# Performance work log

Hardware: AMD Instinct MI355X
Metric: run time of the kernel (lower is better)

Reference implementation:

```python
import jax, jax.numpy as jnp
import numpy as np

T, B, V, L = 512, 32, 512, 128
NEG = -1e9  # safe -inf surrogate (keeps logaddexp gradients finite)


def setup_inputs() -> dict:
    key = jax.random.key(0)
    k1, k2, k3 = jax.random.split(key, 3)
    log_probs = jax.nn.log_softmax(
        jax.random.normal(k1, (T, B, V), dtype=jnp.float32), axis=-1)
    # ASG transition parameter (init ones in the module; use small noise for a
    # non-degenerate reference). transition[i, j] = score of j -> i.
    transition = 0.1 * jax.random.normal(k2, (V, V), dtype=jnp.float32)
    targets = jax.random.randint(k3, (B, L), 0, V)
    input_lengths = jnp.full((B,), T, dtype=jnp.int32)
    target_lengths = jnp.full((B,), L, dtype=jnp.int32)
    return {"log_probs": log_probs, "transition": transition,
            "targets": targets, "input_lengths": input_lengths,
            "target_lengths": target_lengths}


def _fcc(log_probs, transition, input_lengths):
    """Fully-connected criterion: log-partition over all label paths. [B]"""
    def step(alpha, lp_t):  # alpha, lp_t: [B, V]
        # alpha'[b, i] = lp_t[b, i] + logsumexp_j(alpha[b, j] + trans[i, j])
        alpha = lp_t + jax.nn.logsumexp(
            alpha[:, None, :] + transition[None, :, :], axis=2)
        return alpha, jax.nn.logsumexp(alpha, axis=1)

    a0 = log_probs[0]
    _, tail = jax.lax.scan(step, a0, log_probs[1:])
    scores = jnp.concatenate(
        [jax.nn.logsumexp(a0, axis=1)[None], tail], axis=0)  # [T, B]
    return scores[input_lengths - 1, jnp.arange(scores.shape[1])]


def _fac(log_probs, transition, targets, input_lengths, target_lengths):
    """Forced-alignment criterion: DP constrained to the target label seq. [B]"""
    Tt, Bb, _ = log_probs.shape
    Ll = targets.shape[1]
    trans_self = transition[targets, targets]                    # [B, L] stay
    trans_prev = transition[targets[:, 1:], targets[:, :-1]]     # [B, L-1] advance
    # emit[t, b, s] = log_probs[t, b, targets[b, s]]
    emit = jnp.take_along_axis(
        log_probs, jnp.broadcast_to(targets[None], (Tt, Bb, Ll)), axis=2)

    sel = (target_lengths - 1)[:, None]  # [B, 1]

    def final_of(beta):
        return jnp.take_along_axis(beta, sel, axis=1)[:, 0]

    beta0 = jnp.where(jnp.arange(Ll)[None, :] == 0, emit[0], NEG)  # [B, L]

    def step(beta, em_t):
        stay = beta + trans_self
        move = jnp.concatenate(
            [jnp.full((Bb, 1), NEG, beta.dtype),
             beta[:, :-1] + trans_prev], axis=1)
        beta = em_t + jnp.logaddexp(stay, move)
        return beta, final_of(beta)

    _, tail = jax.lax.scan(step, beta0, emit[1:])
    fins = jnp.concatenate([final_of(beta0)[None], tail], axis=0)  # [T, B]
    return fins[input_lengths - 1, jnp.arange(Bb)]


def reference(log_probs, transition, targets, input_lengths, target_lengths):
    # ASG loss (reduction='none'): FCC - FAC, shape [B]
    fcc = _fcc(log_probs, transition, input_lengths)
    fac = _fac(log_probs, transition, targets, input_lengths, target_lengths)
    return fcc - fac
```

## Files before the change

### kernel.cpp

```cpp
#include <hip/hip_runtime.h>
#include <stdint.h>

#define T_ 512
#define B_ 32
#define V_ 512
#define L_ 128
#define NEGF (-1000000000.0f)

#define SE_Q 69.0f
#define SU_Q 127.0f
#define LOGC 9.078313f

typedef int v4i __attribute__((ext_vector_type(4)));

template <int CTRL>
__device__ __forceinline__ int dppmov(int old_, int src) {
    return __builtin_amdgcn_update_dpp(old_, src, CTRL, 0xF, 0xF, false);
}
__device__ __forceinline__ float wave_max64(float x) {
    int xi = __float_as_int(x);
    x = fmaxf(x, __int_as_float(dppmov<0x111>(xi, xi))); xi = __float_as_int(x);
    x = fmaxf(x, __int_as_float(dppmov<0x112>(xi, xi))); xi = __float_as_int(x);
    x = fmaxf(x, __int_as_float(dppmov<0x114>(xi, xi))); xi = __float_as_int(x);
    x = fmaxf(x, __int_as_float(dppmov<0x118>(xi, xi))); xi = __float_as_int(x);
    x = fmaxf(x, __int_as_float(dppmov<0x142>(xi, xi))); xi = __float_as_int(x);
    x = fmaxf(x, __int_as_float(dppmov<0x143>(xi, xi)));
    return x;
}
__device__ __forceinline__ float wave_sum64(float x) {
    int xi = __float_as_int(x);
    x = x + __int_as_float(dppmov<0x111>(xi, xi)); xi = __float_as_int(x);
    x = x + __int_as_float(dppmov<0x112>(xi, xi)); xi = __float_as_int(x);
    x = x + __int_as_float(dppmov<0x114>(xi, xi)); xi = __float_as_int(x);
    x = x + __int_as_float(dppmov<0x118>(xi, xi)); xi = __float_as_int(x);
    x = x + __int_as_float(dppmov<0x142>(xi, xi)); xi = __float_as_int(x);
    x = x + __int_as_float(dppmov<0x143>(xi, xi));
    return x;
}
__device__ __forceinline__ unsigned fkey(float f) {
    unsigned u = __float_as_uint(f);
    return (u & 0x80000000u) ? ~u : (u | 0x80000000u);
}
__device__ __forceinline__ float funkey(unsigned k) {
    unsigned u = (k & 0x80000000u) ? (k ^ 0x80000000u) : ~k;
    return __uint_as_float(u);
}
__device__ __forceinline__ int sel4(v4i a, int r) {
    int x0 = (r & 1) ? a.y : a.x;
    int x1 = (r & 1) ? a.w : a.z;
    return (r & 2) ? x1 : x0;
}

__global__ void asg_prep(const float* __restrict__ trans, uint32_t* __restrict__ Et) {
    int o = blockIdx.x * blockDim.x + threadIdx.x;
    int d    = o & 3;
    int tid  = (o >> 2) & 511;
    int qreg = o >> 11;
    int tt = qreg >> 3, kt = qreg & 7;
    int w = tid >> 6, lane = tid & 63;
    int q = lane >> 4, n = lane & 15;
    int m  = 64 * w + 16 * tt + n;
    int k0 = 64 * kt + 16 * q + 4 * d;
    const float* tp = trans + (size_t)m * V_ + k0;
    uint32_t q0 = (uint32_t)fminf(127.0f, __expf(tp[0]) * SE_Q + 0.5f);
    uint32_t q1 = (uint32_t)fminf(127.0f, __expf(tp[1]) * SE_Q + 0.5f);
    uint32_t q2 = (uint32_t)fminf(127.0f, __expf(tp[2]) * SE_Q + 0.5f);
    uint32_t q3 = (uint32_t)fminf(127.0f, __expf(tp[3]) * SE_Q + 0.5f);
    Et[(size_t)o] = q0 | (q1 << 8) | (q2 << 16) | (q3 << 24);
}

__global__ __attribute__((amdgpu_flat_work_group_size(512, 512),
                          amdgpu_waves_per_eu(2, 2)))
void asg_main(
    const float* __restrict__ lp, const uint32_t* __restrict__ Et,
    const float* __restrict__ trans, const int* __restrict__ targets,
    const int* __restrict__ ilen, const int* __restrict__ tlen,
    float* __restrict__ fcc_ws, float* __restrict__ fac_ws)
{
    __shared__ float facb[256];
    __shared__ __align__(16) uint32_t u_lds[128];
    __shared__ __align__(16) float mw_lds[8];
    __shared__ unsigned mslotE;
    __shared__ float sumf;

    const int bb  = blockIdx.x;
    const int tid = threadIdx.x;

    if (bb < B_) {
        const int b    = bb;
        const int lane = tid & 63;
        const int w    = tid >> 6;
        const int q    = lane >> 4;
        const int n    = lane & 15;
        const int tt_o = n >> 2;
        const int rg_o = n & 3;
        const int i    = 64 * w + 16 * tt_o + 4 * q + rg_o;
        const int Tlen = ilen[b];

        uint4 er4[32];
        {
            const uint4* Eq = (const uint4*)Et;
            #pragma unroll
            for (int t8 = 0; t8 < 32; ++t8) er4[t8] = Eq[t8 * 512 + tid];
        }

        float lpv0 = lp[(size_t)b * V_ + i];
        float elp  = __expf(lpv0);
        float lpv  = lp[(size_t)(B_ * V_) + (size_t)b * V_ + i];
        float accf = 1.0f;
        float S    = 0.0f;
        if (tid == 0) { mslotE = 0u; sumf = 0.0f; }
        __syncthreads();

        for (int t = 1; t < Tlen; ++t) {
            float key   = elp * accf;
            float elp_n = __expf(lpv);

            {
                float mx = wave_max64(key);
                if (lane == 63) mw_lds[w] = mx;
            }
            __syncthreads();

            float4 m0 = *(const float4*)&mw_lds[0];
            float4 m1 = *(const float4*)&mw_lds[4];
            float kmax = fmaxf(fmaxf(fmaxf(m0.x, m0.y), fmaxf(m0.z, m0.w)),
                               fmaxf(fmaxf(m1.x, m1.y), fmaxf(m1.z, m1.w)));
            float r127 = 127.0f * __builtin_amdgcn_rcpf(kmax);

            {
                uint32_t qu = (uint32_t)fminf(127.0f, fmaf(key, r127, 0.5f));
                int pv = (int)(qu << (8 * (i & 3)));
                pv |= dppmov<0xB1>(pv, pv);
                pv |= dppmov<0x4E>(pv, pv);
                if ((i & 3) == 0) u_lds[i >> 2] = (uint32_t)pv;
            }
            __syncthreads();

            uint4 bf[8];
            #pragma unroll
            for (int kt = 0; kt < 8; ++kt)
                bf[kt] = *(const uint4*)((const char*)u_lds + 64 * kt + 16 * q);

            int tn = (t + 1 < Tlen) ? (t + 1) : t;
            float lpv_n = lp[(size_t)tn * (B_ * V_) + (size_t)b * V_ + i];

            v4i a0, a1, a2, a3;
            {
                v4i z = {0, 0, 0, 0};
                a0 = z; a1 = z; a2 = z; a3 = z;
            }
            #pragma unroll
            for (int kt = 0; kt < 8; ++kt) {
                v4i bv = __builtin_bit_cast(v4i, bf[kt]);
                a0 = __builtin_amdgcn_mfma_i32_16x16x64_i8(
                        __builtin_bit_cast(v4i, er4[0 * 8 + kt]), bv, a0, 0, 0, 0);
                a1 = __builtin_amdgcn_mfma_i32_16x16x64_i8(
                        __builtin_bit_cast(v4i, er4[1 * 8 + kt]), bv, a1, 0, 0, 0);
                a2 = __builtin_amdgcn_mfma_i32_16x16x64_i8(
                        __builtin_bit_cast(v4i, er4[2 * 8 + kt]), bv, a2, 0, 0, 0);
                a3 = __builtin_amdgcn_mfma_i32_16x16x64_i8(
                        __builtin_bit_cast(v4i, er4[3 * 8 + kt]), bv, a3, 0, 0, 0);
            }

            int s0 = sel4(a0, rg_o), s1 = sel4(a1, rg_o);
            int s2 = sel4(a2, rg_o), s3 = sel4(a3, rg_o);
            int y0 = (tt_o & 1) ? s1 : s0;
            int y1 = (tt_o & 1) ? s3 : s2;
            int acc = (tt_o & 2) ? y1 : y0;

            accf = (float)acc;
            S += __logf(kmax) - LOGC;
            elp = elp_n;
            lpv = lpv_n;
        }

        float alpha = ((Tlen > 1) ? lpv : lpv0) + S + __logf(accf);
        {
            float mx = wave_max64(alpha);
            if (lane == 63) atomicMax(&mslotE, fkey(mx));
        }
        __syncthreads();
        float m2 = funkey(mslotE);
        {
            float sv = wave_sum64(__expf(alpha - m2));
            if (lane == 63) atomicAdd(&sumf, sv);
        }
        __syncthreads();
        if (tid == 0) fcc_ws[b] = m2 + __logf(sumf);
    } else {
        const int b = bb - B_;
        const int l = tid;
        const bool active = (l < L_);
        const int Tlen = ilen[b];
        const int Llen = tlen[b];

        const int tl  = active ? targets[b * L_ + l] : 0;
        const int tlm = (active && l > 0) ? targets[b * L_ + l - 1] : 0;
        const float ts = active ? trans[(size_t)tl * V_ + tl] : 0.0f;
        const float tp = (active && l > 0) ? trans[(size_t)tl * V_ + tlm] : 0.0f;

        float beta = (l == 0) ? lp[(size_t)b * V_ + tl] : NEGF;
        float em_next = active ? lp[(size_t)1 * (B_ * V_) + (size_t)b * V_ + tl] : 0.0f;

        for (int t = 1; t < Tlen; ++t) {
            float* buf = facb + (t & 1) * L_;
            if (active) buf[l] = beta;
            __syncthreads();
            float prev = (active && l > 0) ? buf[l - 1] : NEGF;
            float em = em_next;
            if (active && t + 1 < Tlen)
                em_next = lp[(size_t)(t + 1) * (B_ * V_) + (size_t)b * V_ + tl];
            if (active) {
                float st = beta + ts;
                float mv = prev + tp;
                float mx = fmaxf(st, mv);
                float mn = fminf(st, mv);
                beta = em + mx + log1pf(__expf(mn - mx));
            }
        }
        if (active && l == Llen - 1) fac_ws[b] = beta;
    }
}

__global__ void asg_combine(const float* __restrict__ fcc_ws,
                            const float* __restrict__ fac_ws,
                            float* __restrict__ out) {
    int i = threadIdx.x;
    if (i < B_) out[i] = fcc_ws[i] - fac_ws[i];
}

extern "C" void kernel_launch(void* const* d_in, const int* in_sizes, int n_in,
                              void* d_out, int out_size, void* d_ws, size_t ws_size,
                              hipStream_t stream) {
    const float* lp      = (const float*)d_in[0];
    const float* trans   = (const float*)d_in[1];
    const int*   targets = (const int*)d_in[2];
    const int*   ilen    = (const int*)d_in[3];
    const int*   tlen    = (const int*)d_in[4];
    float* out = (float*)d_out;

    uint32_t* Et     = (uint32_t*)d_ws;
    float*    fcc_ws = (float*)((char*)d_ws + 65536 * 4);
    float*    fac_ws = fcc_ws + B_;

    hipLaunchKernelGGL(asg_prep, dim3(256), dim3(256), 0, stream, trans, Et);
    hipLaunchKernelGGL(asg_main, dim3(2 * B_), dim3(512), 0, stream,
                       lp, Et, trans, targets, ilen, tlen, fcc_ws, fac_ws);
    hipLaunchKernelGGL(asg_combine, dim3(1), dim3(64), 0, stream, fcc_ws, fac_ws, out);
}
```

Before: 558.7 us.

## Rotate K-tile order per wave and feed own tile via bpermute before barrier

Each wave now processes the K-tiles in a rotated order starting with its own tile. That first tile's B-operand is built directly from registers with ds_bpermute, so the first MFMAs can issue without waiting on the LDS round-trip of the other tiles. The exp of the next log-prob is moved later to overlap with the loads. The aim is to shorten the per-timestep critical path of the serial recurrence, at the cost of extra bpermute instructions and a rotated preload of the E registers.

Measured after the change: 577.7 us. +3.4%, slower.

```diff
diff --git a/kernel.cpp b/kernel.cpp
--- a/kernel.cpp
+++ b/kernel.cpp
@@ -101,7 +101,10 @@
         {
             const uint4* Eq = (const uint4*)Et;
             #pragma unroll
-            for (int t8 = 0; t8 < 32; ++t8) er4[t8] = Eq[t8 * 512 + tid];
+            for (int tt = 0; tt < 4; ++tt)
+                #pragma unroll
+                for (int s = 0; s < 8; ++s)
+                    er4[tt * 8 + s] = Eq[(tt * 8 + ((w + s) & 7)) * 512 + tid];
         }
 
         float lpv0 = lp[(size_t)b * V_ + i];
@@ -113,8 +116,7 @@
         __syncthreads();
 
         for (int t = 1; t < Tlen; ++t) {
-            float key   = elp * accf;
-            float elp_n = __expf(lpv);
+            float key = elp * accf;
 
             {
                 float mx = wave_max64(key);
@@ -128,39 +130,60 @@
                                fmaxf(fmaxf(m1.x, m1.y), fmaxf(m1.z, m1.w)));
             float r127 = 127.0f * __builtin_amdgcn_rcpf(kmax);
 
+            int pv;
             {
                 uint32_t qu = (uint32_t)fminf(127.0f, fmaf(key, r127, 0.5f));
-                int pv = (int)(qu << (8 * (i & 3)));
+                pv = (int)(qu << (8 * (i & 3)));
                 pv |= dppmov<0xB1>(pv, pv);
                 pv |= dppmov<0x4E>(pv, pv);
                 if ((i & 3) == 0) u_lds[i >> 2] = (uint32_t)pv;
             }
+
+            int bbase = lane & 48;
+            int ox = __builtin_amdgcn_ds_bpermute(bbase +   0, pv);
+            int oy = __builtin_amdgcn_ds_bpermute(bbase +  64, pv);
+            int oz = __builtin_amdgcn_ds_bpermute(bbase + 128, pv);
+            int ow = __builtin_amdgcn_ds_bpermute(bbase + 192, pv);
             __syncthreads();
 
-            uint4 bf[8];
+            uint4 bfr[7];
             #pragma unroll
-            for (int kt = 0; kt < 8; ++kt)
-                bf[kt] = *(const uint4*)((const char*)u_lds + 64 * kt + 16 * q);
+            for (int s = 1; s < 8; ++s) {
+                int kt = (w + s) & 7;
+                bfr[s - 1] = *(const uint4*)((const char*)u_lds + 64 * kt + 16 * q);
+            }
 
             int tn = (t + 1 < Tlen) ? (t + 1) : t;
             float lpv_n = lp[(size_t)tn * (B_ * V_) + (size_t)b * V_ + i];
+            float elp_n = __expf(lpv);
 
             v4i a0, a1, a2, a3;
             {
                 v4i z = {0, 0, 0, 0};
                 a0 = z; a1 = z; a2 = z; a3 = z;
             }
+            {
+                v4i bv; bv.x = ox; bv.y = oy; bv.z = oz; bv.w = ow;
+                a0 = __builtin_amdgcn_mfma_i32_16x16x64_i8(
+                        __builtin_bit_cast(v4i, er4[0]),  bv, a0, 0, 0, 0);
+                a1 = __builtin_amdgcn_mfma_i32_16x16x64_i8(
+                        __builtin_bit_cast(v4i, er4[8]),  bv, a1, 0, 0, 0);
+                a2 = __builtin_amdgcn_mfma_i32_16x16x64_i8(
+                        __builtin_bit_cast(v4i, er4[16]), bv, a2, 0, 0, 0);
+                a3 = __builtin_amdgcn_mfma_i32_16x16x64_i8(
+                        __builtin_bit_cast(v4i, er4[24]), bv, a3, 0, 0, 0);
+            }
             #pragma unroll
-            for (int kt = 0; kt < 8; ++kt) {
-                v4i bv = __builtin_bit_cast(v4i, bf[kt]);
+            for (int s = 1; s < 8; ++s) {
+                v4i bv = __builtin_bit_cast(v4i, bfr[s - 1]);
                 a0 = __builtin_amdgcn_mfma_i32_16x16x64_i8(
-                        __builtin_bit_cast(v4i, er4[0 * 8 + kt]), bv, a0, 0, 0, 0);
+                        __builtin_bit_cast(v4i, er4[0 * 8 + s]), bv, a0, 0, 0, 0);
                 a1 = __builtin_amdgcn_mfma_i32_16x16x64_i8(
-                        __builtin_bit_cast(v4i, er4[1 * 8 + kt]), bv, a1, 0, 0, 0);
+                        __builtin_bit_cast(v4i, er4[1 * 8 + s]), bv, a1, 0, 0, 0);
                 a2 = __builtin_amdgcn_mfma_i32_16x16x64_i8(
-                        __builtin_bit_cast(v4i, er4[2 * 8 + kt]), bv, a2, 0, 0, 0);
+                        __builtin_bit_cast(v4i, er4[2 * 8 + s]), bv, a2, 0, 0, 0);
                 a3 = __builtin_amdgcn_mfma_i32_16x16x64_i8(
-                        __builtin_bit_cast(v4i, er4[3 * 8 + kt]), bv, a3, 0, 0, 0);
+                        __builtin_bit_cast(v4i, er4[3 * 8 + s]), bv, a3, 0, 0, 0);
             }
 
             int s0 = sel4(a0, rg_o), s1 = sel4(a1, rg_o);
```

## Use per-wave quantization scale to drop one barrier per FCC step

Applied to the files above, without the earlier changes.

Each wave now quantizes its slice of alpha with its own wave-local max, taken via readlane, instead of a block-wide max. This removes the first __syncthreads per timestep. The per-wave maxima are written to a double-buffered LDS array alongside the packed int8 vector. The int8 MFMA accumulation is split per k-tile so that each 64-wide chunk can be rescaled by its wave's scale relative to the global max in float, which adds extra MFMA result selects and float math per step.

Result: slower. 667.3 us (+19.4%).

```diff
diff --git a/kernel.cpp b/kernel.cpp
--- a/kernel.cpp
+++ b/kernel.cpp
@@ -78,8 +78,8 @@
     float* __restrict__ fcc_ws, float* __restrict__ fac_ws)
 {
     __shared__ float facb[256];
-    __shared__ __align__(16) uint32_t u_lds[128];
-    __shared__ __align__(16) float mw_lds[8];
+    __shared__ __align__(16) uint32_t u_lds[2][128];
+    __shared__ __align__(16) float mw_lds[2][8];
     __shared__ unsigned mslotE;
     __shared__ float sumf;
 
@@ -113,64 +113,73 @@
         __syncthreads();
 
         for (int t = 1; t < Tlen; ++t) {
-            float key   = elp * accf;
-            float elp_n = __expf(lpv);
-
-            {
-                float mx = wave_max64(key);
-                if (lane == 63) mw_lds[w] = mx;
-            }
-            __syncthreads();
-
-            float4 m0 = *(const float4*)&mw_lds[0];
-            float4 m1 = *(const float4*)&mw_lds[4];
-            float kmax = fmaxf(fmaxf(fmaxf(m0.x, m0.y), fmaxf(m0.z, m0.w)),
-                               fmaxf(fmaxf(m1.x, m1.y), fmaxf(m1.z, m1.w)));
-            float r127 = 127.0f * __builtin_amdgcn_rcpf(kmax);
+            const int bi = t & 1;
+            float key = elp * accf;
+
+            float mxw = wave_max64(key);
+            float kmax_w = __int_as_float(
+                __builtin_amdgcn_readlane(__float_as_int(mxw), 63));
+            kmax_w = fmaxf(kmax_w, 1e-30f);
+            float r127 = 127.0f * __builtin_amdgcn_rcpf(kmax_w);
 
             {
                 uint32_t qu = (uint32_t)fminf(127.0f, fmaf(key, r127, 0.5f));
                 int pv = (int)(qu << (8 * (i & 3)));
                 pv |= dppmov<0xB1>(pv, pv);
                 pv |= dppmov<0x4E>(pv, pv);
-                if ((i & 3) == 0) u_lds[i >> 2] = (uint32_t)pv;
+                if ((i & 3) == 0) u_lds[bi][i >> 2] = (uint32_t)pv;
             }
+            if (lane == 63) mw_lds[bi][w] = kmax_w;
+            float elp_n = __expf(lpv);
             __syncthreads();
 
             uint4 bf[8];
             #pragma unroll
             for (int kt = 0; kt < 8; ++kt)
-                bf[kt] = *(const uint4*)((const char*)u_lds + 64 * kt + 16 * q);
+                bf[kt] = *(const uint4*)((const char*)u_lds[bi] + 64 * kt + 16 * q);
+            float4 mv0 = *(const float4*)&mw_lds[bi][0];
+            float4 mv1 = *(const float4*)&mw_lds[bi][4];
 
             int tn = (t + 1 < Tlen) ? (t + 1) : t;
             float lpv_n = lp[(size_t)tn * (B_ * V_) + (size_t)b * V_ + i];
 
-            v4i a0, a1, a2, a3;
+            float kg = fmaxf(fmaxf(fmaxf(mv0.x, mv0.y), fmaxf(mv0.z, mv0.w)),
+                             fmaxf(fmaxf(mv1.x, mv1.y), fmaxf(mv1.z, mv1.w)));
+            float rkg = __builtin_amdgcn_rcpf(kg);
+            float s0 = mv0.x * rkg, s1 = mv0.y * rkg;
+            float s2 = mv0.z * rkg, s3 = mv0.w * rkg;
+            float s4 = mv1.x * rkg, s5 = mv1.y * rkg;
+            float s6 = mv1.z * rkg, s7 = mv1.w * rkg;
+
+            int p[8];
             {
                 v4i z = {0, 0, 0, 0};
-                a0 = z; a1 = z; a2 = z; a3 = z;
+                #pragma unroll
+                for (int kt = 0; kt < 8; ++kt) {
+                    v4i bv = __builtin_bit_cast(v4i, bf[kt]);
+                    v4i a0 = __builtin_amdgcn_mfma_i32_16x16x64_i8(
+                                __builtin_bit_cast(v4i, er4[0 * 8 + kt]), bv, z, 0, 0, 0);
+                    v4i a1 = __builtin_amdgcn_mfma_i32_16x16x64_i8(
+                                __builtin_bit_cast(v4i, er4[1 * 8 + kt]), bv, z, 0, 0, 0);
+                    v4i a2 = __builtin_amdgcn_mfma_i32_16x16x64_i8(
+                                __builtin_bit_cast(v4i, er4[2 * 8 + kt]), bv, z, 0, 0, 0);
+                    v4i a3 = __builtin_amdgcn_mfma_i32_16x16x64_i8(
+                                __builtin_bit_cast(v4i, er4[3 * 8 + kt]), bv, z, 0, 0, 0);
+                    int x0 = sel4(a0, rg_o), x1 = sel4(a1, rg_o);
+                    int x2 = sel4(a2, rg_o), x3 = sel4(a3, rg_o);
+                    int y0 = (tt_o & 1) ? x1 : x0;
+                    int y1 = (tt_o & 1) ? x3 : x2;
+                    p[kt] = (tt_o & 2) ? y1 : y0;
+                }
             }
-            #pragma unroll
-            for (int kt = 0; kt < 8; ++kt) {
-                v4i bv = __builtin_bit_cast(v4i, bf[kt]);
-                a0 = __builtin_amdgcn_mfma_i32_16x16x64_i8(
-                        __builtin_bit_cast(v4i, er4[0 * 8 + kt]), bv, a0, 0, 0, 0);
-                a1 = __builtin_amdgcn_mfma_i32_16x16x64_i8(
-                        __builtin_bit_cast(v4i, er4[1 * 8 + kt]), bv, a1, 0, 0, 0);
-                a2 = __builtin_amdgcn_mfma_i32_16x16x64_i8(
-                        __builtin_bit_cast(v4i, er4[2 * 8 + kt]), bv, a2, 0, 0, 0);
-                a3 = __builtin_amdgcn_mfma_i32_16x16x64_i8(
-                        __builtin_bit_cast(v4i, er4[3 * 8 + kt]), bv, a3, 0, 0, 0);
-            }
-
-            int s0 = sel4(a0, rg_o), s1 = sel4(a1, rg_o);
-            int s2 = sel4(a2, rg_o), s3 = sel4(a3, rg_o);
-            int y0 = (tt_o & 1) ? s1 : s0;
-            int y1 = (tt_o & 1) ? s3 : s2;
-            int acc = (tt_o & 2) ? y1 : y0;
-
-            accf = (float)acc;
-            S += __logf(kmax) - LOGC;
+
+            float t0 = fmaf(s0, (float)p[0], s1 * (float)p[1]);
+            float t1 = fmaf(s2, (float)p[2], s3 * (float)p[3]);
+            float t2 = fmaf(s4, (float)p[4], s5 * (float)p[5]);
+            float t3 = fmaf(s6, (float)p[6], s7 * (float)p[7]);
+            accf = (t0 + t1) + (t2 + t3);
+
+            S += __logf(kg) - LOGC;
             elp = elp_n;
             lpv = lpv_n;
         }
```
